# Kernel optimization log

Measured on AMD Instinct MI355X. Metric: run time of the kernel, lower is better.

Reference implementation:

```python
import jax, jax.numpy as jnp
import numpy as np

H = 1024   # hidden_dim
NH = 16    # num_heads
HD = H // NH  # head_dim = 64
B, S = 2, 2048
LN_EPS = 1e-5


def setup_inputs() -> dict:
    key = jax.random.key(0)
    ks = jax.random.split(key, 5)
    scale = 1.0 / np.sqrt(H)  # xavier-ish scale for stability
    return {
        "x": jax.random.normal(ks[0], (B, S, H), dtype=jnp.float32),
        "Wq": jax.random.normal(ks[1], (H, H), dtype=jnp.float32) * scale,
        "bq": jnp.zeros((H,), jnp.float32),
        "Wk": jax.random.normal(ks[2], (H, H), dtype=jnp.float32) * scale,
        "bk": jnp.zeros((H,), jnp.float32),
        "Wv": jax.random.normal(ks[3], (H, H), dtype=jnp.float32) * scale,
        "bv": jnp.zeros((H,), jnp.float32),
        "Wo": jax.random.normal(ks[4], (H, H), dtype=jnp.float32) * scale,
        "bo": jnp.zeros((H,), jnp.float32),
        "ln_gamma": jnp.ones((H,), jnp.float32),
        "ln_beta": jnp.zeros((H,), jnp.float32),
    }


def reference(x, Wq, bq, Wk, bk, Wv, bv, Wo, bo, ln_gamma, ln_beta):
    b, s, _ = x.shape
    # QKV projections, split heads: (b, nh, s, hd)
    def split_heads(t):
        return t.reshape(b, s, NH, HD).transpose(0, 2, 1, 3)
    Q = split_heads(x @ Wq + bq)
    K = split_heads(x @ Wk + bk)
    V = split_heads(x @ Wv + bv)
    # scaled dot-product with clamp (mask=None path)
    scores = jnp.einsum('bhqd,bhkd->bhqk', Q, K) / np.sqrt(HD).astype(np.float32)
    scores = jnp.clip(scores, -10000.0, 10000.0)
    attn = jax.nn.softmax(scores, axis=-1)
    # dropout is identity in eval mode
    ctx = jnp.einsum('bhqk,bhkd->bhqd', attn, V)
    ctx = ctx.transpose(0, 2, 1, 3).reshape(b, s, H)
    out = ctx @ Wo + bo
    # residual + LayerNorm
    y = out + x
    mu = jnp.mean(y, axis=-1, keepdims=True)
    var = jnp.mean(jnp.square(y - mu), axis=-1, keepdims=True)
    y = (y - mu) * jax.lax.rsqrt(var + LN_EPS)
    return y * ln_gamma + ln_beta
```

## Files before the change

### kernel.cpp

```cpp
#include <hip/hip_runtime.h>

typedef unsigned short u16;
typedef __attribute__((ext_vector_type(8))) short shortx8;
typedef __attribute__((ext_vector_type(4))) float floatx4;
typedef __attribute__((ext_vector_type(2))) float floatx2;
typedef __attribute__((ext_vector_type(2))) unsigned uintx2;
typedef __attribute__((ext_vector_type(4))) unsigned uintx4;

#define GLD16(gp, lp) __builtin_amdgcn_global_load_lds( \
    (__attribute__((address_space(1))) void*)(gp), \
    (__attribute__((address_space(3))) void*)(lp), 16, 0, 0)

#define BAR() __builtin_amdgcn_s_barrier()
#define LGKM0() do { asm volatile("s_waitcnt lgkmcnt(0)" ::: "memory"); \
                     __builtin_amdgcn_sched_barrier(0); } while (0)
#define VMCNT0() do { asm volatile("s_waitcnt vmcnt(0)" ::: "memory"); \
                      __builtin_amdgcn_sched_barrier(0); } while (0)

__device__ __forceinline__ u16 f2bf(float f) {
  union { float f; unsigned u; } v; v.f = f;
  unsigned r = v.u + 0x7FFFu + ((v.u >> 16) & 1u);
  return (u16)(r >> 16);
}

__device__ __forceinline__ unsigned pkbf(float a, float b) {
#if __has_builtin(__builtin_amdgcn_cvt_pk_bf16_f32)
  auto r = __builtin_amdgcn_cvt_pk_bf16_f32(a, b);
  return __builtin_bit_cast(unsigned, r);
#else
  union { float f; unsigned u; } x, y; x.f = a; y.f = b;
  return __builtin_amdgcn_perm(y.u + 0x8000u, x.u + 0x8000u, 0x07060302u);
#endif
}

__global__ __launch_bounds__(256) void prep_kernel(const float* __restrict__ x,
                                                   u16* __restrict__ xb,
                                                   const float* __restrict__ Wq,
                                                   const float* __restrict__ Wk,
                                                   const float* __restrict__ Wv,
                                                   const float* __restrict__ Wo,
                                                   u16* __restrict__ Wt) {
  __shared__ u16 tile[32][33];
  int bid = blockIdx.x;
  int tid = threadIdx.x;
  if (bid < 4096) {
    int i = bid * 256 + tid;
    float4 v = ((const float4*)x)[i];
    uintx2 o;
    o.x = pkbf(v.x, v.y);
    o.y = pkbf(v.z, v.w);
    ((uintx2*)xb)[i] = o;
  } else {
    int block = bid - 4096;
    int mat = block >> 10;
    int rem = block & 1023;
    const float* W = (mat == 0) ? Wq : (mat == 1) ? Wk : (mat == 2) ? Wv : Wo;
    u16* dst = Wt + (size_t)mat * 1024 * 1024;
    int n0 = (rem & 31) * 32, k0 = (rem >> 5) * 32;
    int tx = tid & 31, ty = tid >> 5;
    for (int i = 0; i < 4; ++i)
      tile[ty + i * 8][tx] = f2bf(W[(size_t)(k0 + ty + i * 8) * 1024 + n0 + tx]);
    __syncthreads();
    for (int i = 0; i < 4; ++i)
      dst[(size_t)(n0 + ty + i * 8) * 1024 + k0 + tx] = tile[tx][ty + i * 8];
  }
}

__global__ __launch_bounds__(256, 2) void qkv_gemm(const u16* __restrict__ xb,
                                                   const u16* __restrict__ Wt,
                                                   const float* __restrict__ bq,
                                                   const float* __restrict__ bk,
                                                   const float* __restrict__ bv,
                                                   u16* __restrict__ Qh,
                                                   u16* __restrict__ Kh,
                                                   u16* __restrict__ Vth) {
  __shared__ u16 lds[32768];
  const int tid = threadIdx.x;
  const int wave = tid >> 6, lane = tid & 63;
  const int lrow = lane >> 4, lcol = lane & 15;
  const int wm = wave >> 1, wn = wave & 1;
  const int m0 = blockIdx.x * 128;
  const int nt = blockIdx.y;
  const int mat = nt >> 3;
  const int n0 = (nt & 7) * 128;
  const u16* Ag = xb;
  const u16* Bg = Wt + (size_t)mat * 1048576;

  const u16* sa[4];
  const u16* sb[4];
#pragma unroll
  for (int l = 0; l < 4; ++l) {
    int g = (l * 4 + wave) * 64 + lane;
    int r = g >> 3, c = g & 7;
    int cc = (c ^ (r & 7)) * 8;
    sa[l] = Ag + (size_t)(m0 + r) * 1024 + cc;
    sb[l] = Bg + (size_t)(n0 + r) * 1024 + cc;
  }

  floatx4 acc[4][4];
#pragma unroll
  for (int mi = 0; mi < 4; ++mi)
#pragma unroll
    for (int ni = 0; ni < 4; ++ni)
      acc[mi][ni] = (floatx4){0.f, 0.f, 0.f, 0.f};

#pragma unroll
  for (int l = 0; l < 4; ++l) {
    GLD16(sa[l], lds + (l * 4 + wave) * 512);
    GLD16(sb[l], lds + 8192 + (l * 4 + wave) * 512);
  }
  VMCNT0();
  BAR();

#pragma unroll 2
  for (int t = 0; t < 16; ++t) {
    const int rb = t & 1, wb = rb ^ 1;
    const u16* Ab = lds + rb * 16384;
    const u16* Bb = lds + rb * 16384 + 8192;
    u16* Aw = lds + wb * 16384;
    u16* Bw = lds + wb * 16384 + 8192;
    const int k64 = (t + 1) * 64;

    if (t < 15) {
#pragma unroll
      for (int l = 0; l < 4; ++l) GLD16(sa[l] + k64, Aw + (l * 4 + wave) * 512);
    }
    shortx8 bfr[4][2];
#pragma unroll
    for (int ni = 0; ni < 4; ++ni) {
      int rn = wn * 64 + ni * 16 + lcol;
#pragma unroll
      for (int kk = 0; kk < 2; ++kk)
        bfr[ni][kk] = *(const shortx8*)&Bb[rn * 64 + (((kk * 4 + lrow) ^ (rn & 7)) * 8)];
    }
    {
      shortx8 afr[2][2];
#pragma unroll
      for (int j = 0; j < 2; ++j) {
        int rm = wm * 64 + j * 16 + lcol;
#pragma unroll
        for (int kk = 0; kk < 2; ++kk)
          afr[j][kk] = *(const shortx8*)&Ab[rm * 64 + (((kk * 4 + lrow) ^ (rm & 7)) * 8)];
      }
      BAR();
      LGKM0();
      __builtin_amdgcn_s_setprio(1);
#pragma unroll
      for (int kk = 0; kk < 2; ++kk)
#pragma unroll
        for (int j = 0; j < 2; ++j)
#pragma unroll
          for (int ni = 0; ni < 4; ++ni)
            acc[j][ni] = __builtin_amdgcn_mfma_f32_16x16x32_bf16(
                afr[j][kk], bfr[ni][kk], acc[j][ni], 0, 0, 0);
      __builtin_amdgcn_s_setprio(0);
      BAR();
    }
    if (t < 15) {
#pragma unroll
      for (int l = 0; l < 4; ++l) GLD16(sb[l] + k64, Bw + (l * 4 + wave) * 512);
    }
    {
      shortx8 afr[2][2];
#pragma unroll
      for (int j = 0; j < 2; ++j) {
        int rm = wm * 64 + (2 + j) * 16 + lcol;
#pragma unroll
        for (int kk = 0; kk < 2; ++kk)
          afr[j][kk] = *(const shortx8*)&Ab[rm * 64 + (((kk * 4 + lrow) ^ (rm & 7)) * 8)];
      }
      BAR();
      LGKM0();
      __builtin_amdgcn_s_setprio(1);
#pragma unroll
      for (int kk = 0; kk < 2; ++kk)
#pragma unroll
        for (int j = 0; j < 2; ++j)
#pragma unroll
          for (int ni = 0; ni < 4; ++ni)
            acc[2 + j][ni] = __builtin_amdgcn_mfma_f32_16x16x32_bf16(
                afr[j][kk], bfr[ni][kk], acc[2 + j][ni], 0, 0, 0);
      __builtin_amdgcn_s_setprio(0);
      VMCNT0();
      BAR();
    }
  }

  const float* bias = (mat == 0) ? bq : (mat == 1) ? bk : bv;
  const float qscale = 0.18033688011f;

  if (mat < 2) {
    u16* dst = (mat == 0) ? Qh : Kh;
    float sc = (mat == 0) ? qscale : 1.0f;
#pragma unroll
    for (int mi = 0; mi < 4; ++mi) {
      int mb = wm * 64 + mi * 16 + lrow * 4;
#pragma unroll
      for (int ni = 0; ni < 4; ++ni) {
        int n = wn * 64 + ni * 16 + lcol;
        float bval = bias[n0 + n];
#pragma unroll
        for (int r = 0; r < 4; ++r) {
          int m = mb + r;
          lds[m * 128 + (((n >> 3) ^ (m & 15)) * 8) + (n & 7)] =
              f2bf((acc[mi][ni][r] + bval) * sc);
        }
      }
    }
    __syncthreads();
    int row = tid >> 1, half = tid & 1;
    int m = m0 + row;
    int bb = m >> 11, s = m & 2047;
#pragma unroll
    for (int i = 0; i < 8; ++i) {
      int cg = half * 8 + i;
      int pg = cg ^ (row & 15);
      shortx8 v = *(const shortx8*)&lds[row * 128 + pg * 8];
      int ng = n0 + cg * 8;
      int hh = ng >> 6, d = ng & 63;
      *(shortx8*)&dst[((size_t)(bb * 16 + hh) * 2048 + s) * 64 + d] = v;
    }
  } else {
#pragma unroll
    for (int mi = 0; mi < 4; ++mi) {
      int mbase = m0 + wm * 64 + mi * 16 + lrow * 4;
      int bb = mbase >> 11, s = mbase & 2047;
#pragma unroll
      for (int ni = 0; ni < 4; ++ni) {
        int n = n0 + wn * 64 + ni * 16 + lcol;
        float bval = bias[n];
        int hh = n >> 6, d = n & 63;
        uintx2 pk;
        pk.x = pkbf(acc[mi][ni][0] + bval, acc[mi][ni][1] + bval);
        pk.y = pkbf(acc[mi][ni][2] + bval, acc[mi][ni][3] + bval);
        *(uintx2*)&Vth[((size_t)(bb * 16 + hh) * 64 + d) * 2048 + s] = pk;
      }
    }
  }
}

__global__ __launch_bounds__(256, 2) void out_gemm(const u16* __restrict__ ctx,
                                                   const u16* __restrict__ Wot,
                                                   const float* __restrict__ bo,
                                                   float* __restrict__ aout) {
  __shared__ u16 lds[24576];
  const int tid = threadIdx.x;
  const int wave = tid >> 6, lane = tid & 63;
  const int lrow = lane >> 4, lcol = lane & 15;
  const int wm = wave >> 1, wn = wave & 1;
  const int m0 = blockIdx.x * 128;
  const int n0 = blockIdx.y * 64;

  const u16* sa[4];
  const u16* sb[2];
#pragma unroll
  for (int l = 0; l < 4; ++l) {
    int g = (l * 4 + wave) * 64 + lane;
    int r = g >> 3, c = g & 7;
    sa[l] = ctx + (size_t)(m0 + r) * 1024 + ((c ^ (r & 7)) * 8);
  }
#pragma unroll
  for (int l = 0; l < 2; ++l) {
    int g = (l * 4 + wave) * 64 + lane;
    int r = g >> 3, c = g & 7;
    sb[l] = Wot + (size_t)(n0 + r) * 1024 + ((c ^ (r & 7)) * 8);
  }

  floatx4 acc[4][2];
#pragma unroll
  for (int mi = 0; mi < 4; ++mi)
#pragma unroll
    for (int ni = 0; ni < 2; ++ni)
      acc[mi][ni] = (floatx4){0.f, 0.f, 0.f, 0.f};

#pragma unroll
  for (int l = 0; l < 4; ++l) GLD16(sa[l], lds + (l * 4 + wave) * 512);
#pragma unroll
  for (int l = 0; l < 2; ++l) GLD16(sb[l], lds + 8192 + (l * 4 + wave) * 512);
  VMCNT0();
  BAR();

#pragma unroll 2
  for (int t = 0; t < 16; ++t) {
    const int rb = t & 1, wb = rb ^ 1;
    const u16* Ab = lds + rb * 12288;
    const u16* Bb = lds + rb * 12288 + 8192;
    u16* Aw = lds + wb * 12288;
    u16* Bw = lds + wb * 12288 + 8192;
    const int k64 = (t + 1) * 64;

    if (t < 15) {
#pragma unroll
      for (int l = 0; l < 4; ++l) GLD16(sa[l] + k64, Aw + (l * 4 + wave) * 512);
    }
    shortx8 bfr[2][2];
#pragma unroll
    for (int ni = 0; ni < 2; ++ni) {
      int rn = wn * 32 + ni * 16 + lcol;
#pragma unroll
      for (int kk = 0; kk < 2; ++kk)
        bfr[ni][kk] = *(const shortx8*)&Bb[rn * 64 + (((kk * 4 + lrow) ^ (rn & 7)) * 8)];
    }
    {
      shortx8 afr[2][2];
#pragma unroll
      for (int j = 0; j < 2; ++j) {
        int rm = wm * 64 + j * 16 + lcol;
#pragma unroll
        for (int kk = 0; kk < 2; ++kk)
          afr[j][kk] = *(const shortx8*)&Ab[rm * 64 + (((kk * 4 + lrow) ^ (rm & 7)) * 8)];
      }
      BAR();
      LGKM0();
      __builtin_amdgcn_s_setprio(1);
#pragma unroll
      for (int kk = 0; kk < 2; ++kk)
#pragma unroll
        for (int j = 0; j < 2; ++j)
#pragma unroll
          for (int ni = 0; ni < 2; ++ni)
            acc[j][ni] = __builtin_amdgcn_mfma_f32_16x16x32_bf16(
                afr[j][kk], bfr[ni][kk], acc[j][ni], 0, 0, 0);
      __builtin_amdgcn_s_setprio(0);
      BAR();
    }
    if (t < 15) {
#pragma unroll
      for (int l = 0; l < 2; ++l) GLD16(sb[l] + k64, Bw + (l * 4 + wave) * 512);
    }
    {
      shortx8 afr[2][2];
#pragma unroll
      for (int j = 0; j < 2; ++j) {
        int rm = wm * 64 + (2 + j) * 16 + lcol;
#pragma unroll
        for (int kk = 0; kk < 2; ++kk)
          afr[j][kk] = *(const shortx8*)&Ab[rm * 64 + (((kk * 4 + lrow) ^ (rm & 7)) * 8)];
      }
      BAR();
      LGKM0();
      __builtin_amdgcn_s_setprio(1);
#pragma unroll
      for (int kk = 0; kk < 2; ++kk)
#pragma unroll
        for (int j = 0; j < 2; ++j)
#pragma unroll
          for (int ni = 0; ni < 2; ++ni)
            acc[2 + j][ni] = __builtin_amdgcn_mfma_f32_16x16x32_bf16(
                afr[j][kk], bfr[ni][kk], acc[2 + j][ni], 0, 0, 0);
      __builtin_amdgcn_s_setprio(0);
      VMCNT0();
      BAR();
    }
  }

#pragma unroll
  for (int mi = 0; mi < 4; ++mi) {
    int mbase = m0 + wm * 64 + mi * 16 + lrow * 4;
#pragma unroll
    for (int ni = 0; ni < 2; ++ni) {
      int n = n0 + wn * 32 + ni * 16 + lcol;
      float bval = bo[n];
#pragma unroll
      for (int r = 0; r < 4; ++r)
        aout[(size_t)(mbase + r) * 1024 + n] = acc[mi][ni][r] + bval;
    }
  }
}

__global__ __launch_bounds__(512) void attn_kernel(const u16* __restrict__ Qh,
                                                   const u16* __restrict__ Kh,
                                                   const u16* __restrict__ Vth,
                                                   u16* __restrict__ ctx) {
  __shared__ u16 QPs[128 * 64];
  __shared__ u16 Ks[2][64 * 64];
  __shared__ u16 Vs[2][64 * 64];

  int bh = blockIdx.x;
  int b = bh >> 4, h = bh & 15;
  int q0 = blockIdx.y * 128;
  int tid = threadIdx.x;
  int wave = tid >> 6, lane = tid & 63;
  int lrow = lane >> 4, lcol = lane & 15;

  const u16* Qg = Qh + ((size_t)bh * 2048 + q0) * 64;
  for (int l = 0; l < 2; ++l) {
    int g = (l * 8 + wave) * 64 + lane;
    int r = g >> 3, c = g & 7;
    GLD16(Qg + r * 64 + ((c ^ (r & 7)) * 8), QPs + (l * 8 + wave) * 512);
  }

  const u16* Kbase = Kh + (size_t)bh * 2048 * 64;
  const u16* Vbase = Vth + (size_t)bh * 64 * 2048;

  int g = wave * 64 + lane;
  int gr = g >> 3, gc = g & 7;
  int cc = (gc ^ (gr & 7)) * 8;
  const u16* kp = Kbase + (size_t)gr * 64 + cc;

  const u16* vp = Vbase + (size_t)gr * 2048 + gc * 8;
  int hh = gc >> 2, ct = gc & 3;
  int ua = 4 * (ct & 1) + (ct >> 1);
  int chunkA = hh * 4 + (ua >> 1);
  int offA = gr * 128 + ((chunkA ^ (gr & 7)) * 16) + (ua & 1) * 8;
  int offB = gr * 128 + (((chunkA + 1) ^ (gr & 7)) * 16) + (ua & 1) * 8;

  {
    float4 vreg = *(const float4*)vp;
    vp += 64;
    GLD16(kp, (u16*)Ks + wave * 512);
    kp += 4096;
    char* vb = (char*)Vs;
    *(floatx2*)(vb + offA) = (floatx2){vreg.x, vreg.y};
    *(floatx2*)(vb + offB) = (floatx2){vreg.z, vreg.w};
  }
  __syncthreads();

  shortx8 qf[2];
  for (int kk = 0; kk < 2; ++kk) {
    int row = wave * 16 + lcol;
    int grr = (kk * 4 + lrow) ^ (row & 7);
    qf[kk] = *(const shortx8*)&QPs[row * 64 + grr * 8];
  }

  const short one_bf = (short)0x3F80;
  const shortx8 ones8 = {one_bf, one_bf, one_bf, one_bf, one_bf, one_bf, one_bf, one_bf};

  floatx4 o[4];
  floatx4 lacc = (floatx4){0.f, 0.f, 0.f, 0.f};
  for (int dt = 0; dt < 4; ++dt) o[dt] = (floatx4){0.f, 0.f, 0.f, 0.f};

  for (int i = 0; i < 32; ++i) {
    int cur = i & 1;
    float4 vreg;
    if (i < 31) {
      vreg = *(const float4*)vp;
      vp += 64;
      GLD16(kp, (u16*)Ks + (cur ^ 1) * 4096 + wave * 512);
      kp += 4096;
    }

    floatx4 sc[4];
    for (int kt = 0; kt < 4; ++kt)
      sc[kt] = (floatx4){0.f, 0.f, 0.f, 0.f};
    __builtin_amdgcn_s_setprio(1);
    for (int kk = 0; kk < 2; ++kk) {
      for (int kt = 0; kt < 4; ++kt) {
        int row = kt * 16 + lcol;
        int grr = (kk * 4 + lrow) ^ (row & 7);
        shortx8 kf = *(const shortx8*)&Ks[cur][row * 64 + grr * 8];
        sc[kt] = __builtin_amdgcn_mfma_f32_16x16x32_bf16(kf, qf[kk], sc[kt], 0, 0, 0);
      }
    }
    __builtin_amdgcn_s_setprio(0);

    float p[4][4];
    for (int kt = 0; kt < 4; ++kt)
      for (int r = 0; r < 4; ++r)
        p[kt][r] = __builtin_amdgcn_exp2f(sc[kt][r]);
    shortx8 pf[2];
    for (int kk = 0; kk < 2; ++kk) {
      uintx4 w;
      w.x = pkbf(p[2 * kk][0], p[2 * kk][1]);
      w.y = pkbf(p[2 * kk][2], p[2 * kk][3]);
      w.z = pkbf(p[2 * kk + 1][0], p[2 * kk + 1][1]);
      w.w = pkbf(p[2 * kk + 1][2], p[2 * kk + 1][3]);
      pf[kk] = __builtin_bit_cast(shortx8, w);
    }

    if (i < 31) {
      char* vb = (char*)Vs + (cur ^ 1) * 8192;
      *(floatx2*)(vb + offA) = (floatx2){vreg.x, vreg.y};
      *(floatx2*)(vb + offB) = (floatx2){vreg.z, vreg.w};
    }

    __builtin_amdgcn_s_setprio(1);
    for (int kk = 0; kk < 2; ++kk) {
      lacc = __builtin_amdgcn_mfma_f32_16x16x32_bf16(ones8, pf[kk], lacc, 0, 0, 0);
      for (int dt = 0; dt < 4; ++dt) {
        int row = dt * 16 + lcol;
        int grr = (kk * 4 + lrow) ^ (row & 7);
        shortx8 vf = *(const shortx8*)&Vs[cur][row * 64 + grr * 8];
        o[dt] = __builtin_amdgcn_mfma_f32_16x16x32_bf16(vf, pf[kk], o[dt], 0, 0, 0);
      }
    }
    __builtin_amdgcn_s_setprio(0);
    __syncthreads();
  }

  {
    float inv = 1.0f / lacc[0];
    int s = q0 + wave * 16 + lcol;
    u16* dst = ctx + (size_t)(b * 2048 + s) * 1024 + h * 64 + lrow * 4;
    for (int dt = 0; dt < 4; ++dt) {
      uintx2 pk;
      pk.x = pkbf(o[dt][0] * inv, o[dt][1] * inv);
      pk.y = pkbf(o[dt][2] * inv, o[dt][3] * inv);
      *(uintx2*)(dst + dt * 16) = pk;
    }
  }
}

__global__ __launch_bounds__(256) void ln_kernel(const float* __restrict__ aout,
                                                 const float* __restrict__ x,
                                                 const float* __restrict__ gamma,
                                                 const float* __restrict__ beta,
                                                 float* __restrict__ out) {
  int row = blockIdx.x;
  int t = threadIdx.x;
  const float4* a4 = (const float4*)(aout + (size_t)row * 1024);
  const float4* x4 = (const float4*)(x + (size_t)row * 1024);
  float4 v = a4[t];
  float4 xv = x4[t];
  v.x += xv.x; v.y += xv.y; v.z += xv.z; v.w += xv.w;
  float s = v.x + v.y + v.z + v.w;
  float s2 = v.x * v.x + v.y * v.y + v.z * v.z + v.w * v.w;
  for (int off = 1; off < 64; off <<= 1) {
    s += __shfl_xor(s, off, 64);
    s2 += __shfl_xor(s2, off, 64);
  }
  __shared__ float red[8];
  int wave = t >> 6, lane = t & 63;
  if (lane == 0) { red[wave] = s; red[4 + wave] = s2; }
  __syncthreads();
  s = red[0] + red[1] + red[2] + red[3];
  s2 = red[4] + red[5] + red[6] + red[7];
  float mu = s * (1.0f / 1024.0f);
  float var = s2 * (1.0f / 1024.0f) - mu * mu;
  float rstd = rsqrtf(var + 1e-5f);
  float4 g = ((const float4*)gamma)[t];
  float4 be = ((const float4*)beta)[t];
  float4 y;
  y.x = (v.x - mu) * rstd * g.x + be.x;
  y.y = (v.y - mu) * rstd * g.y + be.y;
  y.z = (v.z - mu) * rstd * g.z + be.z;
  y.w = (v.w - mu) * rstd * g.w + be.w;
  ((float4*)(out + (size_t)row * 1024))[t] = y;
}

extern "C" void kernel_launch(void* const* d_in, const int* in_sizes, int n_in,
                              void* d_out, int out_size, void* d_ws, size_t ws_size,
                              hipStream_t stream) {
  const float* x     = (const float*)d_in[0];
  const float* Wq    = (const float*)d_in[1];
  const float* bq    = (const float*)d_in[2];
  const float* Wk    = (const float*)d_in[3];
  const float* bk    = (const float*)d_in[4];
  const float* Wv    = (const float*)d_in[5];
  const float* bv    = (const float*)d_in[6];
  const float* Wo    = (const float*)d_in[7];
  const float* bo    = (const float*)d_in[8];
  const float* gamma = (const float*)d_in[9];
  const float* beta  = (const float*)d_in[10];
  float* out = (float*)d_out;

  char* ws = (char*)d_ws;
  u16* xb   = (u16*)(ws);
  u16* Wt   = (u16*)(ws + ((size_t)8 << 20));
  u16* Qh   = (u16*)(ws + ((size_t)16 << 20));
  u16* Kh   = (u16*)(ws + ((size_t)24 << 20));
  u16* Vth  = (u16*)(ws + ((size_t)32 << 20));
  u16* ctx  = (u16*)(ws + ((size_t)40 << 20));
  float* aout = (float*)(ws + ((size_t)48 << 20));

  prep_kernel<<<8192, 256, 0, stream>>>(x, xb, Wq, Wk, Wv, Wo, Wt);
  qkv_gemm<<<dim3(32, 24), 256, 0, stream>>>(xb, Wt, bq, bk, bv, Qh, Kh, Vth);
  attn_kernel<<<dim3(32, 16), 512, 0, stream>>>(Qh, Kh, Vth, ctx);
  out_gemm<<<dim3(32, 16), 256, 0, stream>>>(ctx, Wt + (size_t)3 * 1024 * 1024, bo, aout);
  ln_kernel<<<4096, 256, 0, stream>>>(aout, x, gamma, beta, out);
}
```

Before: 196.3 us.

## Retile QKV GEMM to 256x192 blocks with 8 waves over fused N

The QKV projection GEMM moves from 128x128 tiles with 4 waves (768 blocks) to 256x192 tiles with 8 waves (256 blocks, one per CU). The N dimension now spans the concatenated Q/K/V weights, so a tile can straddle matrix boundaries, and the epilogue selects the destination and bias per column. The intent is to reuse A and B more per LDS load and to run one full wave of blocks matching the CU count. The cost is more LDS (128KB), one block per CU with lower occupancy, and more barriers per k-step from the four sub-phases.

```diff
diff --git a/kernel.cpp b/kernel.cpp
--- a/kernel.cpp
+++ b/kernel.cpp
@@ -66,7 +66,7 @@
   }
 }
 
-__global__ __launch_bounds__(256, 2) void qkv_gemm(const u16* __restrict__ xb,
+__global__ __launch_bounds__(512, 1) void qkv_gemm(const u16* __restrict__ xb,
                                                    const u16* __restrict__ Wt,
                                                    const float* __restrict__ bq,
                                                    const float* __restrict__ bk,
@@ -74,61 +74,62 @@
                                                    u16* __restrict__ Qh,
                                                    u16* __restrict__ Kh,
                                                    u16* __restrict__ Vth) {
-  __shared__ u16 lds[32768];
+  __shared__ u16 lds[65536];
   const int tid = threadIdx.x;
   const int wave = tid >> 6, lane = tid & 63;
   const int lrow = lane >> 4, lcol = lane & 15;
-  const int wm = wave >> 1, wn = wave & 1;
-  const int m0 = blockIdx.x * 128;
-  const int nt = blockIdx.y;
-  const int mat = nt >> 3;
-  const int n0 = (nt & 7) * 128;
+  const int wm = wave >> 2, wn = wave & 3;
+  const int m0 = blockIdx.x * 256;
+  const int n0 = blockIdx.y * 192;
   const u16* Ag = xb;
-  const u16* Bg = Wt + (size_t)mat * 1048576;
+  const u16* Bg = Wt;
 
   const u16* sa[4];
-  const u16* sb[4];
+  const u16* sb[3];
 #pragma unroll
   for (int l = 0; l < 4; ++l) {
-    int g = (l * 4 + wave) * 64 + lane;
+    int g = (l * 8 + wave) * 64 + lane;
     int r = g >> 3, c = g & 7;
-    int cc = (c ^ (r & 7)) * 8;
-    sa[l] = Ag + (size_t)(m0 + r) * 1024 + cc;
-    sb[l] = Bg + (size_t)(n0 + r) * 1024 + cc;
-  }
-
-  floatx4 acc[4][4];
-#pragma unroll
-  for (int mi = 0; mi < 4; ++mi)
-#pragma unroll
-    for (int ni = 0; ni < 4; ++ni)
+    sa[l] = Ag + (size_t)(m0 + r) * 1024 + ((c ^ (r & 7)) * 8);
+  }
+#pragma unroll
+  for (int l = 0; l < 3; ++l) {
+    int g = (l * 8 + wave) * 64 + lane;
+    int r = g >> 3, c = g & 7;
+    sb[l] = Bg + (size_t)(n0 + r) * 1024 + ((c ^ (r & 7)) * 8);
+  }
+
+  floatx4 acc[8][3];
+#pragma unroll
+  for (int mi = 0; mi < 8; ++mi)
+#pragma unroll
+    for (int ni = 0; ni < 3; ++ni)
       acc[mi][ni] = (floatx4){0.f, 0.f, 0.f, 0.f};
 
 #pragma unroll
-  for (int l = 0; l < 4; ++l) {
-    GLD16(sa[l], lds + (l * 4 + wave) * 512);
-    GLD16(sb[l], lds + 8192 + (l * 4 + wave) * 512);
-  }
+  for (int l = 0; l < 4; ++l) GLD16(sa[l], lds + (l * 8 + wave) * 512);
+#pragma unroll
+  for (int l = 0; l < 3; ++l) GLD16(sb[l], lds + 16384 + (l * 8 + wave) * 512);
   VMCNT0();
   BAR();
 
 #pragma unroll 2
   for (int t = 0; t < 16; ++t) {
     const int rb = t & 1, wb = rb ^ 1;
-    const u16* Ab = lds + rb * 16384;
-    const u16* Bb = lds + rb * 16384 + 8192;
-    u16* Aw = lds + wb * 16384;
-    u16* Bw = lds + wb * 16384 + 8192;
+    const u16* Ab = lds + rb * 28672;
+    const u16* Bb = lds + rb * 28672 + 16384;
+    u16* Aw = lds + wb * 28672;
+    u16* Bw = lds + wb * 28672 + 16384;
     const int k64 = (t + 1) * 64;
 
     if (t < 15) {
 #pragma unroll
-      for (int l = 0; l < 4; ++l) GLD16(sa[l] + k64, Aw + (l * 4 + wave) * 512);
-    }
-    shortx8 bfr[4][2];
-#pragma unroll
-    for (int ni = 0; ni < 4; ++ni) {
-      int rn = wn * 64 + ni * 16 + lcol;
+      for (int l = 0; l < 4; ++l) GLD16(sa[l] + k64, Aw + (l * 8 + wave) * 512);
+    }
+    shortx8 bfr[3][2];
+#pragma unroll
+    for (int ni = 0; ni < 3; ++ni) {
+      int rn = wn * 48 + ni * 16 + lcol;
 #pragma unroll
       for (int kk = 0; kk < 2; ++kk)
         bfr[ni][kk] = *(const shortx8*)&Bb[rn * 64 + (((kk * 4 + lrow) ^ (rn & 7)) * 8)];
@@ -137,7 +138,7 @@
       shortx8 afr[2][2];
 #pragma unroll
       for (int j = 0; j < 2; ++j) {
-        int rm = wm * 64 + j * 16 + lcol;
+        int rm = wm * 128 + j * 16 + lcol;
 #pragma unroll
         for (int kk = 0; kk < 2; ++kk)
           afr[j][kk] = *(const shortx8*)&Ab[rm * 64 + (((kk * 4 + lrow) ^ (rm & 7)) * 8)];
@@ -150,7 +151,7 @@
 #pragma unroll
         for (int j = 0; j < 2; ++j)
 #pragma unroll
-          for (int ni = 0; ni < 4; ++ni)
+          for (int ni = 0; ni < 3; ++ni)
             acc[j][ni] = __builtin_amdgcn_mfma_f32_16x16x32_bf16(
                 afr[j][kk], bfr[ni][kk], acc[j][ni], 0, 0, 0);
       __builtin_amdgcn_s_setprio(0);
@@ -158,13 +159,13 @@
     }
     if (t < 15) {
 #pragma unroll
-      for (int l = 0; l < 4; ++l) GLD16(sb[l] + k64, Bw + (l * 4 + wave) * 512);
+      for (int l = 0; l < 3; ++l) GLD16(sb[l] + k64, Bw + (l * 8 + wave) * 512);
     }
     {
       shortx8 afr[2][2];
 #pragma unroll
       for (int j = 0; j < 2; ++j) {
-        int rm = wm * 64 + (2 + j) * 16 + lcol;
+        int rm = wm * 128 + (2 + j) * 16 + lcol;
 #pragma unroll
         for (int kk = 0; kk < 2; ++kk)
           afr[j][kk] = *(const shortx8*)&Ab[rm * 64 + (((kk * 4 + lrow) ^ (rm & 7)) * 8)];
@@ -177,64 +178,109 @@
 #pragma unroll
         for (int j = 0; j < 2; ++j)
 #pragma unroll
-          for (int ni = 0; ni < 4; ++ni)
+          for (int ni = 0; ni < 3; ++ni)
             acc[2 + j][ni] = __builtin_amdgcn_mfma_f32_16x16x32_bf16(
                 afr[j][kk], bfr[ni][kk], acc[2 + j][ni], 0, 0, 0);
       __builtin_amdgcn_s_setprio(0);
+      BAR();
+    }
+    {
+      shortx8 afr[2][2];
+#pragma unroll
+      for (int j = 0; j < 2; ++j) {
+        int rm = wm * 128 + (4 + j) * 16 + lcol;
+#pragma unroll
+        for (int kk = 0; kk < 2; ++kk)
+          afr[j][kk] = *(const shortx8*)&Ab[rm * 64 + (((kk * 4 + lrow) ^ (rm & 7)) * 8)];
+      }
+      BAR();
+      LGKM0();
+      __builtin_amdgcn_s_setprio(1);
+#pragma unroll
+      for (int kk = 0; kk < 2; ++kk)
+#pragma unroll
+        for (int j = 0; j < 2; ++j)
+#pragma unroll
+          for (int ni = 0; ni < 3; ++ni)
+            acc[4 + j][ni] = __builtin_amdgcn_mfma_f32_16x16x32_bf16(
+                afr[j][kk], bfr[ni][kk], acc[4 + j][ni], 0, 0, 0);
+      __builtin_amdgcn_s_setprio(0);
+      BAR();
+    }
+    {
+      shortx8 afr[2][2];
+#pragma unroll
+      for (int j = 0; j < 2; ++j) {
+        int rm = wm * 128 + (6 + j) * 16 + lcol;
+#pragma unroll
+        for (int kk = 0; kk < 2; ++kk)
+          afr[j][kk] = *(const shortx8*)&Ab[rm * 64 + (((kk * 4 + lrow) ^ (rm & 7)) * 8)];
+      }
+      BAR();
+      LGKM0();
+      __builtin_amdgcn_s_setprio(1);
+#pragma unroll
+      for (int kk = 0; kk < 2; ++kk)
+#pragma unroll
+        for (int j = 0; j < 2; ++j)
+#pragma unroll
+          for (int ni = 0; ni < 3; ++ni)
+            acc[6 + j][ni] = __builtin_amdgcn_mfma_f32_16x16x32_bf16(
+                afr[j][kk], bfr[ni][kk], acc[6 + j][ni], 0, 0, 0);
+      __builtin_amdgcn_s_setprio(0);
       VMCNT0();
       BAR();
     }
   }
 
-  const float* bias = (mat == 0) ? bq : (mat == 1) ? bk : bv;
   const float qscale = 0.18033688011f;
-
-  if (mat < 2) {
-    u16* dst = (mat == 0) ? Qh : Kh;
-    float sc = (mat == 0) ? qscale : 1.0f;
-#pragma unroll
-    for (int mi = 0; mi < 4; ++mi) {
-      int mb = wm * 64 + mi * 16 + lrow * 4;
-#pragma unroll
-      for (int ni = 0; ni < 4; ++ni) {
-        int n = wn * 64 + ni * 16 + lcol;
-        float bval = bias[n0 + n];
+  __syncthreads();
+
+#pragma unroll
+  for (int mi = 0; mi < 8; ++mi) {
+    int mb = wm * 128 + mi * 16 + lrow * 4;
+#pragma unroll
+    for (int ni = 0; ni < 3; ++ni) {
+      int nl = wn * 48 + ni * 16 + lcol;
+      int ng = n0 + nl;
+      int mt = ng >> 10;
+      if (mt < 2) {
+        float sc = (mt == 0) ? qscale : 1.0f;
+        float bval = ((mt == 0) ? bq : bk)[ng & 1023] * sc;
 #pragma unroll
         for (int r = 0; r < 4; ++r) {
           int m = mb + r;
-          lds[m * 128 + (((n >> 3) ^ (m & 15)) * 8) + (n & 7)] =
-              f2bf((acc[mi][ni][r] + bval) * sc);
+          lds[m * 256 + (((nl >> 3) ^ (m & 31)) * 8) + (nl & 7)] =
+              f2bf(acc[mi][ni][r] * sc + bval);
         }
-      }
-    }
-    __syncthreads();
-    int row = tid >> 1, half = tid & 1;
-    int m = m0 + row;
-    int bb = m >> 11, s = m & 2047;
-#pragma unroll
-    for (int i = 0; i < 8; ++i) {
-      int cg = half * 8 + i;
-      int pg = cg ^ (row & 15);
-      shortx8 v = *(const shortx8*)&lds[row * 128 + pg * 8];
-      int ng = n0 + cg * 8;
-      int hh = ng >> 6, d = ng & 63;
-      *(shortx8*)&dst[((size_t)(bb * 16 + hh) * 2048 + s) * 64 + d] = v;
-    }
-  } else {
-#pragma unroll
-    for (int mi = 0; mi < 4; ++mi) {
-      int mbase = m0 + wm * 64 + mi * 16 + lrow * 4;
-      int bb = mbase >> 11, s = mbase & 2047;
-#pragma unroll
-      for (int ni = 0; ni < 4; ++ni) {
-        int n = n0 + wn * 64 + ni * 16 + lcol;
-        float bval = bias[n];
-        int hh = n >> 6, d = n & 63;
+      } else {
+        float bval = bv[ng & 1023];
+        int mbase = m0 + mb;
+        int bb = mbase >> 11, s = mbase & 2047;
+        int hh = (ng & 1023) >> 6, d = ng & 63;
         uintx2 pk;
         pk.x = pkbf(acc[mi][ni][0] + bval, acc[mi][ni][1] + bval);
         pk.y = pkbf(acc[mi][ni][2] + bval, acc[mi][ni][3] + bval);
         *(uintx2*)&Vth[((size_t)(bb * 16 + hh) * 64 + d) * 2048 + s] = pk;
       }
+    }
+  }
+  __syncthreads();
+  {
+    int row = tid >> 1, half = tid & 1;
+    int m = m0 + row;
+    int bb = m >> 11, s = m & 2047;
+#pragma unroll
+    for (int i = 0; i < 12; ++i) {
+      int cg = half * 12 + i;
+      int ng = n0 + cg * 8;
+      int mt = ng >> 10;
+      if (mt >= 2) continue;
+      u16* dst = (mt == 0) ? Qh : Kh;
+      int pg = cg ^ (row & 31);
+      shortx8 v = *(const shortx8*)&lds[row * 256 + pg * 8];
+      int hh = (ng & 1023) >> 6, d = ng & 63;
+      *(shortx8*)&dst[((size_t)(bb * 16 + hh) * 2048 + s) * 64 + d] = v;
     }
   }
 }
@@ -564,7 +610,7 @@
   float* aout = (float*)(ws + ((size_t)48 << 20));
 
   prep_kernel<<<8192, 256, 0, stream>>>(x, xb, Wq, Wk, Wv, Wo, Wt);
-  qkv_gemm<<<dim3(32, 24), 256, 0, stream>>>(xb, Wt, bq, bk, bv, Qh, Kh, Vth);
+  qkv_gemm<<<dim3(16, 16), 512, 0, stream>>>(xb, Wt, bq, bk, bv, Qh, Kh, Vth);
   attn_kernel<<<dim3(32, 16), 512, 0, stream>>>(Qh, Kh, Vth, ctx);
   out_gemm<<<dim3(32, 16), 256, 0, stream>>>(ctx, Wt + (size_t)3 * 1024 * 1024, bo, aout);
   ln_kernel<<<4096, 256, 0, stream>>>(aout, x, gamma, beta, out);
```

Result: no change. 195.5 us (-0.4%).
